# Optimization experiments

Hardware: AMD Instinct MI355X
Metric: run time of the kernel (lower is better)

## Reference

```python
import math
import jax, jax.numpy as jnp
import numpy as np

FS = 96000.0
N_BIQUADS = 16
HPF_FREQ_RANGE = (20.0, 500.0)
LPF_FREQ_RANGE = (5000.0, 20000.0)
SHELF_FREQ_RANGE = (50.0, 16000.0)
PEAK_FREQ_RANGE = (100.0, 15000.0)
Q_RANGE = (0.5, 16.0)
GAIN_RANGE = (-24.0, 24.0)
BROADBAND_RANGE = (-60.0, 0.0)


def _denorm_log(norm, lo, hi):
    return jnp.exp(math.log(lo) + norm * (math.log(hi) - math.log(lo)))


def _coef_highpass(fc, Q):
    w0 = 2.0 * math.pi * fc / FS
    alpha = jnp.sin(w0) / (2.0 * Q)
    c = jnp.cos(w0)
    b0 = (1 + c) / 2; b1 = -(1 + c); b2 = (1 + c) / 2
    a0 = 1 + alpha; a1 = -2 * c; a2 = 1 - alpha
    return b0 / a0, b1 / a0, b2 / a0, a1 / a0, a2 / a0


def _coef_lowpass(fc, Q):
    w0 = 2.0 * math.pi * fc / FS
    alpha = jnp.sin(w0) / (2.0 * Q)
    c = jnp.cos(w0)
    b0 = (1 - c) / 2; b1 = 1 - c; b2 = (1 - c) / 2
    a0 = 1 + alpha; a1 = -2 * c; a2 = 1 - alpha
    return b0 / a0, b1 / a0, b2 / a0, a1 / a0, a2 / a0


def _coef_lowshelf(fc, gain_db, Q):
    A = 10.0 ** (gain_db / 40.0)
    w0 = 2.0 * math.pi * fc / FS
    alpha = jnp.sin(w0) / (2.0 * Q)
    c = jnp.cos(w0)
    sA = jnp.sqrt(A)
    b0 = A * (A + 1 - (A - 1) * c + 2 * sA * alpha)
    b1 = 2 * A * (A - 1 - (A + 1) * c)
    b2 = A * (A + 1 - (A - 1) * c - 2 * sA * alpha)
    a0 = A + 1 + (A - 1) * c + 2 * sA * alpha
    a1 = -2 * (A - 1 + (A + 1) * c)
    a2 = A + 1 + (A - 1) * c - 2 * sA * alpha
    return b0 / a0, b1 / a0, b2 / a0, a1 / a0, a2 / a0


def _coef_highshelf(fc, gain_db, Q):
    A = 10.0 ** (gain_db / 40.0)
    w0 = 2.0 * math.pi * fc / FS
    alpha = jnp.sin(w0) / (2.0 * Q)
    c = jnp.cos(w0)
    sA = jnp.sqrt(A)
    b0 = A * (A + 1 + (A - 1) * c + 2 * sA * alpha)
    b1 = -2 * A * (A - 1 + (A + 1) * c)
    b2 = A * (A + 1 + (A - 1) * c - 2 * sA * alpha)
    a0 = A + 1 - (A - 1) * c + 2 * sA * alpha
    a1 = 2 * (A - 1 - (A + 1) * c)
    a2 = A + 1 - (A - 1) * c - 2 * sA * alpha
    return b0 / a0, b1 / a0, b2 / a0, a1 / a0, a2 / a0


def _coef_peak(fc, gain_db, Q):
    A = 10.0 ** (gain_db / 40.0)
    w0 = 2.0 * math.pi * fc / FS
    alpha = jnp.sin(w0) / (2.0 * Q)
    c = jnp.cos(w0)
    b0 = 1 + alpha * A; b1 = -2 * c; b2 = 1 - alpha * A
    a0 = 1 + alpha / A; a1 = -2 * c; a2 = 1 - alpha / A
    return b0 / a0, b1 / a0, b2 / a0, a1 / a0, a2 / a0


def _biquad(x, coefs):
    # x: (B, T); coefs: 5 arrays of shape (B,)
    b0, b1, b2, a1, a2 = coefs

    def step(carry, xt):  # xt: (B,)
        s1, s2 = carry
        y = b0 * xt + s1
        return (b1 * xt - a1 * y + s2, b2 * xt - a2 * y), y

    z = jnp.zeros(x.shape[0], x.dtype)
    _, ys = jax.lax.scan(step, (z, z), x.T)  # ys: (T, B)
    return ys.T


def _chain(audio, params):
    B = audio.shape[0]
    bp = params[:, :N_BIQUADS * 3].reshape(B, N_BIQUADS, 3)
    bb_lo, bb_hi = BROADBAND_RANGE
    in_db = bb_lo + params[:, -2] * (bb_hi - bb_lo)
    out_db = bb_lo + params[:, -1] * (bb_hi - bb_lo)
    x = audio * (10.0 ** (in_db / 20.0))[:, None]

    for i in range(N_BIQUADS):
        fn, gn, qn = bp[:, i, 0], bp[:, i, 1], bp[:, i, 2]
        Q = _denorm_log(qn, *Q_RANGE)
        gain = GAIN_RANGE[0] + gn * (GAIN_RANGE[1] - GAIN_RANGE[0])
        if i == 0:  # HPF
            coefs = _coef_highpass(_denorm_log(fn, *HPF_FREQ_RANGE), Q)
        elif i == 15:  # LPF
            coefs = _coef_lowpass(_denorm_log(fn, *LPF_FREQ_RANGE), Q)
        elif i == 1:  # low shelf
            coefs = _coef_lowshelf(_denorm_log(fn, *SHELF_FREQ_RANGE), gain, Q)
        elif i == 14:  # high shelf
            coefs = _coef_highshelf(_denorm_log(fn, *SHELF_FREQ_RANGE), gain, Q)
        else:  # peaking EQ
            coefs = _coef_peak(_denorm_log(fn, *PEAK_FREQ_RANGE), gain, Q)
        x = _biquad(x, coefs)

    return x * (10.0 ** (out_db / 20.0))[:, None]


def setup_inputs() -> dict:
    key = jax.random.key(0)
    k1, k2 = jax.random.split(key)
    audio = jax.random.normal(k1, (16, 262144), dtype=jnp.float32)
    params = jax.random.uniform(k2, (16, 50), dtype=jnp.float32)
    return {"audio": audio, "params": params}


def reference(audio, params):
    return _chain(audio, params)
```

## Files before the change

kernel.cpp:

```cpp
#include <hip/hip_runtime.h>
#include <math.h>

#define BATCH   16
#define T_LEN   262144
#define NB      16
#define L       64
#define GRP     64
#define SUB     16
#define CHAINS  4
#define NSUB    256
#define NSUP    16
#define NG      64
#define NCHUNK  4096

#define DPI 3.14159265358979323846264338327950288

#define OFF_COEF  0
#define OFF_A64   1536
#define OFF_A1K   17920
#define OFF_A16K  34304
#define OFF_QEND  50688
#define OFF_SARR  181760
#define OFF_P     312832

__device__ inline void stage_coefs(int i, double fn, double gn, double qn,
                                   double& B0, double& B1, double& B2,
                                   double& A1, double& A2) {
    const double FS = 96000.0;
    double Q    = exp(log(0.5) + qn * (log(16.0) - log(0.5)));
    double gain = -24.0 + gn * 48.0;
    double lo, hi;
    if (i == 0)            { lo = 20.0;   hi = 500.0;   }
    else if (i == 15)      { lo = 5000.0; hi = 20000.0; }
    else if (i == 1 || i == 14) { lo = 50.0; hi = 16000.0; }
    else                   { lo = 100.0;  hi = 15000.0; }
    double fc    = exp(log(lo) + fn * (log(hi) - log(lo)));
    double w0    = 2.0 * DPI * fc / FS;
    double alpha = sin(w0) / (2.0 * Q);
    double c     = cos(w0);
    double b0, b1, b2, a0, a1, a2;
    if (i == 0) {
        b0 = (1.0 + c) * 0.5; b1 = -(1.0 + c); b2 = (1.0 + c) * 0.5;
        a0 = 1.0 + alpha; a1 = -2.0 * c; a2 = 1.0 - alpha;
    } else if (i == 15) {
        b0 = (1.0 - c) * 0.5; b1 = 1.0 - c; b2 = (1.0 - c) * 0.5;
        a0 = 1.0 + alpha; a1 = -2.0 * c; a2 = 1.0 - alpha;
    } else if (i == 1) {
        double A = pow(10.0, gain / 40.0), sA = sqrt(A);
        b0 = A * ((A + 1.0) - (A - 1.0) * c + 2.0 * sA * alpha);
        b1 = 2.0 * A * ((A - 1.0) - (A + 1.0) * c);
        b2 = A * ((A + 1.0) - (A - 1.0) * c - 2.0 * sA * alpha);
        a0 = (A + 1.0) + (A - 1.0) * c + 2.0 * sA * alpha;
        a1 = -2.0 * ((A - 1.0) + (A + 1.0) * c);
        a2 = (A + 1.0) + (A - 1.0) * c - 2.0 * sA * alpha;
    } else if (i == 14) {
        double A = pow(10.0, gain / 40.0), sA = sqrt(A);
        b0 = A * ((A + 1.0) + (A - 1.0) * c + 2.0 * sA * alpha);
        b1 = -2.0 * A * ((A - 1.0) + (A + 1.0) * c);
        b2 = A * ((A + 1.0) + (A - 1.0) * c - 2.0 * sA * alpha);
        a0 = (A + 1.0) - (A - 1.0) * c + 2.0 * sA * alpha;
        a1 = 2.0 * ((A - 1.0) - (A + 1.0) * c);
        a2 = (A + 1.0) - (A - 1.0) * c - 2.0 * sA * alpha;
    } else {
        double A = pow(10.0, gain / 40.0);
        b0 = 1.0 + alpha * A; b1 = -2.0 * c; b2 = 1.0 - alpha * A;
        a0 = 1.0 + alpha / A; a1 = -2.0 * c; a2 = 1.0 - alpha / A;
    }
    B0 = b0 / a0; B1 = b1 / a0; B2 = b2 / a0; A1 = a1 / a0; A2 = a2 / a0;
}

__global__ __launch_bounds__(256) void k0_setup(const float* __restrict__ params,
                                                float* __restrict__ coefs,
                                                float* __restrict__ A64,
                                                float* __restrict__ A1K,
                                                float* __restrict__ A16K) {
    int b = blockIdx.x;
    int t = threadIdx.x;
    __shared__ double cf[NB][5];
    __shared__ double M1[32 * 32];
    __shared__ double M2[32 * 32];

    if (t < NB) {
        double B0, B1, B2, A1, A2;
        stage_coefs(t, (double)params[b * 50 + t * 3 + 0],
                       (double)params[b * 50 + t * 3 + 1],
                       (double)params[b * 50 + t * 3 + 2], B0, B1, B2, A1, A2);
        float f0 = (float)B0, f1 = (float)B1, f2 = (float)B2, f3 = (float)A1, f4 = (float)A2;
        cf[t][0] = (double)f0; cf[t][1] = (double)f1; cf[t][2] = (double)f2;
        cf[t][3] = (double)f3; cf[t][4] = (double)f4;
        float* cp = coefs + b * 96 + t * 5;
        cp[0] = f0; cp[1] = f1; cp[2] = f2; cp[3] = f3; cp[4] = f4;
    }
    if (t == NB) {
        double indb = -60.0 + (double)params[b * 50 + 48] * 60.0;
        coefs[b * 96 + 80] = (float)pow(10.0, indb / 20.0);
    }
    if (t == NB + 1) {
        double outdb = -60.0 + (double)params[b * 50 + 49] * 60.0;
        coefs[b * 96 + 81] = (float)pow(10.0, outdb / 20.0);
    }
    __syncthreads();

    if (t < 32) {
        double s1[NB], s2[NB];
#pragma unroll
        for (int i = 0; i < NB; i++) {
            s1[i] = (t == 2 * i) ? 1.0 : 0.0;
            s2[i] = (t == 2 * i + 1) ? 1.0 : 0.0;
        }
        double u = 0.0;
#pragma unroll
        for (int i = 0; i < NB; i++) {
            double y  = cf[i][0] * u + s1[i];
            double n1 = cf[i][1] * u - cf[i][3] * y + s2[i];
            double n2 = cf[i][2] * u - cf[i][4] * y;
            s1[i] = n1; s2[i] = n2; u = y;
        }
#pragma unroll
        for (int i = 0; i < NB; i++) {
            M1[(2 * i) * 32 + t]     = s1[i];
            M1[(2 * i + 1) * 32 + t] = s2[i];
        }
    }
    __syncthreads();

    int c  = t & 31;
    int r0 = t >> 5;
    double* src = M1;
    double* dst = M2;
    for (int sq = 0; sq < 14; sq++) {
        double acc[4] = {0.0, 0.0, 0.0, 0.0};
        for (int k = 0; k < 32; k++) {
            double bv = src[k * 32 + c];
#pragma unroll
            for (int e = 0; e < 4; e++)
                acc[e] += src[(e * 8 + r0) * 32 + k] * bv;
        }
#pragma unroll
        for (int e = 0; e < 4; e++) dst[(e * 8 + r0) * 32 + c] = acc[e];
        __syncthreads();
        { double* tmp = src; src = dst; dst = tmp; }
        float* out_m = (sq == 5) ? A64 : (sq == 9) ? A1K : (sq == 13) ? A16K : nullptr;
        if (out_m) {
#pragma unroll
            for (int e = 0; e < 4; e++) {
                int idx = (e * 8 + r0) * 32 + c;
                out_m[b * 1024 + idx] = (float)src[idx];
            }
        }
        __syncthreads();
    }
}

__device__ __forceinline__ float mv_step_rl(const float* ar, float q, float addv) {
    int qi = __float_as_int(q);
    float qb[32];
#pragma unroll
    for (int t = 0; t < 32; t++)
        qb[t] = __int_as_float(__builtin_amdgcn_readlane(qi, t));
    float acc0 = addv, acc1 = 0.f;
#pragma unroll
    for (int t = 0; t < 32; t += 2) {
        acc0 = fmaf(ar[t], qb[t], acc0);
        acc1 = fmaf(ar[t + 1], qb[t + 1], acc1);
    }
    return acc0 + acc1;
}

__device__ __forceinline__ void load_row32(const float* base, int row, float* ar) {
    const float4* a4 = (const float4*)(base + row * 32);
#pragma unroll
    for (int j = 0; j < 8; j++) {
        float4 v = a4[j];
        ar[4 * j + 0] = v.x; ar[4 * j + 1] = v.y;
        ar[4 * j + 2] = v.z; ar[4 * j + 3] = v.w;
    }
}

__device__ __forceinline__ void biquad4(const float4& xc, float ing,
                                        const float* c0, const float* c1,
                                        const float* c2, const float* c3,
                                        const float* c4,
                                        float* s1, float* s2, float* ys) {
    float xs[4] = {xc.x, xc.y, xc.z, xc.w};
#pragma unroll
    for (int j = 0; j < 4; j++) {
        float u = ing * xs[j];
#pragma unroll
        for (int i = 0; i < NB; i++) {
            float y  = fmaf(c0[i], u, s1[i]);
            float n1 = fmaf(c1[i], u, s2[i]); n1 = fmaf(-c3[i], y, n1);
            float n2 = c2[i] * u;             n2 = fmaf(-c4[i], y, n2);
            s1[i] = n1; s2[i] = n2; u = y;
        }
        ys[j] = u;
    }
}

__global__ __launch_bounds__(64, 4) void k1_pass1(const float* __restrict__ audio,
                                                  const float* __restrict__ coefs,
                                                  const float* __restrict__ A64,
                                                  float* __restrict__ P,
                                                  float* __restrict__ Qend) {
    int blk   = blockIdx.x;
    int batch = blk >> 6;
    int grp   = blk & 63;
    int lane  = threadIdx.x;
    int row   = lane & 31;

    __shared__ float plds[GRP][33];

    const float* cf = coefs + batch * 96;
    float c0[NB], c1[NB], c2[NB], c3[NB], c4[NB];
#pragma unroll
    for (int i = 0; i < NB; i++) {
        c0[i] = cf[i * 5 + 0]; c1[i] = cf[i * 5 + 1]; c2[i] = cf[i * 5 + 2];
        c3[i] = cf[i * 5 + 3]; c4[i] = cf[i * 5 + 4];
    }
    float ing = cf[80];

    float s1[NB], s2[NB];
#pragma unroll
    for (int i = 0; i < NB; i++) { s1[i] = 0.f; s2[i] = 0.f; }

    const float4* xgv = (const float4*)(audio + (size_t)batch * T_LEN
                                        + ((size_t)grp * GRP + lane) * L);
    float ys[4];
    float4 xv = xgv[0];
#pragma unroll 1
    for (int tt = 0; tt < 15; tt++) {
        float4 xc = xv;
        xv = xgv[tt + 1];
        biquad4(xc, ing, c0, c1, c2, c3, c4, s1, s2, ys);
    }
    biquad4(xv, ing, c0, c1, c2, c3, c4, s1, s2, ys);

    {
        float* pb = P + ((size_t)(batch * NG + grp)) * 2048;
#pragma unroll
        for (int i = 0; i < NB; i++) {
            pb[(2 * i) * 64 + lane]     = s1[i];
            pb[(2 * i + 1) * 64 + lane] = s2[i];
        }
    }

#pragma unroll
    for (int i = 0; i < NB; i++) {
        plds[lane][2 * i]     = s1[i];
        plds[lane][2 * i + 1] = s2[i];
    }
    __syncthreads();

    float ar[32];
    load_row32(A64 + batch * 1024, row, ar);
    float q0 = 0.f, q1 = 0.f, q2 = 0.f, q3 = 0.f;
#pragma unroll 1
    for (int j = 0; j < SUB; j++) {
        float p0 = plds[0 * SUB + j][row];
        float p1 = plds[1 * SUB + j][row];
        float p2 = plds[2 * SUB + j][row];
        float p3 = plds[3 * SUB + j][row];
        q0 = mv_step_rl(ar, q0, p0);
        q1 = mv_step_rl(ar, q1, p1);
        q2 = mv_step_rl(ar, q2, p2);
        q3 = mv_step_rl(ar, q3, p3);
    }
    if (lane < 32) {
        float* qe = Qend + ((size_t)(batch * NSUB + grp * CHAINS)) * 32 + row;
        qe[0] = q0; qe[32] = q1; qe[64] = q2; qe[96] = q3;
    }
}

__global__ __launch_bounds__(256, 1) void k2_combine(const float* __restrict__ A1K,
                                                     const float* __restrict__ A16K,
                                                     const float* __restrict__ Qend,
                                                     float* __restrict__ Sarr) {
    int batch = blockIdx.x;
    int tid   = threadIdx.x;
    int wave  = tid >> 6;
    int lane  = tid & 63;
    int row   = lane & 31;

    __shared__ float qe[NSUB][32];
    __shared__ float qs[NSUP][32];
    __shared__ float ss[NSUP][32];

    {
        const float4* src4 = (const float4*)(Qend + (size_t)batch * NSUB * 32);
        float4* dst4 = (float4*)&qe[0][0];
        for (int i = tid; i < NSUB * 32 / 4; i += 256) dst4[i] = src4[i];
    }
    float ar1k[32];
    load_row32(A1K + batch * 1024, row, ar1k);
    __syncthreads();

    int s0i = wave * 4;
    {
        float q0 = 0.f, q1 = 0.f, q2 = 0.f, q3 = 0.f;
#pragma unroll 1
        for (int j = 0; j < 16; j++) {
            float p0 = qe[(s0i + 0) * 16 + j][row];
            float p1 = qe[(s0i + 1) * 16 + j][row];
            float p2 = qe[(s0i + 2) * 16 + j][row];
            float p3 = qe[(s0i + 3) * 16 + j][row];
            q0 = mv_step_rl(ar1k, q0, p0);
            q1 = mv_step_rl(ar1k, q1, p1);
            q2 = mv_step_rl(ar1k, q2, p2);
            q3 = mv_step_rl(ar1k, q3, p3);
        }
        if (lane < 32) {
            qs[s0i + 0][row] = q0; qs[s0i + 1][row] = q1;
            qs[s0i + 2][row] = q2; qs[s0i + 3][row] = q3;
        }
    }
    __syncthreads();

    if (wave == 0) {
        float ark[32];
        load_row32(A16K + batch * 1024, row, ark);
        float S = 0.f;
#pragma unroll 1
        for (int s = 0; s < NSUP; s++) {
            if (lane < 32) ss[s][row] = S;
            float addv = qs[s][row];
            S = mv_step_rl(ark, S, addv);
        }
    }
    __syncthreads();

    {
        float q0 = ss[s0i + 0][row];
        float q1 = ss[s0i + 1][row];
        float q2 = ss[s0i + 2][row];
        float q3 = ss[s0i + 3][row];
#pragma unroll 1
        for (int j = 0; j < 16; j++) {
            if (lane < 32) {
                Sarr[((size_t)(batch * NSUB + (s0i + 0) * 16 + j)) * 32 + row] = q0;
                Sarr[((size_t)(batch * NSUB + (s0i + 1) * 16 + j)) * 32 + row] = q1;
                Sarr[((size_t)(batch * NSUB + (s0i + 2) * 16 + j)) * 32 + row] = q2;
                Sarr[((size_t)(batch * NSUB + (s0i + 3) * 16 + j)) * 32 + row] = q3;
            }
            float p0 = qe[(s0i + 0) * 16 + j][row];
            float p1 = qe[(s0i + 1) * 16 + j][row];
            float p2 = qe[(s0i + 2) * 16 + j][row];
            float p3 = qe[(s0i + 3) * 16 + j][row];
            q0 = mv_step_rl(ar1k, q0, p0);
            q1 = mv_step_rl(ar1k, q1, p1);
            q2 = mv_step_rl(ar1k, q2, p2);
            q3 = mv_step_rl(ar1k, q3, p3);
        }
    }
}

__global__ __launch_bounds__(64, 4) void k3_pass2(const float* __restrict__ audio,
                                                  const float* __restrict__ coefs,
                                                  const float* __restrict__ A64,
                                                  const float* __restrict__ P,
                                                  const float* __restrict__ Sarr,
                                                  float* __restrict__ out) {
    int blk   = blockIdx.x;
    int batch = blk >> 6;
    int grp   = blk & 63;
    int lane  = threadIdx.x;
    int row   = lane & 31;

    __shared__ float plds[GRP][33];

    {
        const float* pb = P + ((size_t)(batch * NG + grp)) * 2048;
        float pv[32];
#pragma unroll
        for (int s = 0; s < 32; s++) pv[s] = pb[s * 64 + lane];
#pragma unroll
        for (int s = 0; s < 32; s++) plds[lane][s] = pv[s];
    }
    __syncthreads();

    {
        float ar[32];
        load_row32(A64 + batch * 1024, row, ar);
        const float* sp = Sarr + ((size_t)(batch * NSUB + grp * CHAINS)) * 32 + row;
        float q0 = sp[0], q1 = sp[32], q2 = sp[64], q3 = sp[96];
#pragma unroll 1
        for (int j = 0; j < SUB; j++) {
            float p0 = plds[0 * SUB + j][row];
            float p1 = plds[1 * SUB + j][row];
            float p2 = plds[2 * SUB + j][row];
            float p3 = plds[3 * SUB + j][row];
            if (lane < 32) {
                plds[0 * SUB + j][row] = q0;
                plds[1 * SUB + j][row] = q1;
                plds[2 * SUB + j][row] = q2;
                plds[3 * SUB + j][row] = q3;
            }
            q0 = mv_step_rl(ar, q0, p0);
            q1 = mv_step_rl(ar, q1, p1);
            q2 = mv_step_rl(ar, q2, p2);
            q3 = mv_step_rl(ar, q3, p3);
        }
    }
    __syncthreads();

    const float* cf = coefs + batch * 96;
    float c0[NB], c1[NB], c2[NB], c3[NB], c4[NB];
#pragma unroll
    for (int i = 0; i < NB; i++) {
        c0[i] = cf[i * 5 + 0]; c1[i] = cf[i * 5 + 1]; c2[i] = cf[i * 5 + 2];
        c3[i] = cf[i * 5 + 3]; c4[i] = cf[i * 5 + 4];
    }
    float ing  = cf[80];
    float outg = cf[81];

    float s1[NB], s2[NB];
#pragma unroll
    for (int i = 0; i < NB; i++) {
        s1[i] = plds[lane][2 * i];
        s2[i] = plds[lane][2 * i + 1];
    }

    const float4* xgv = (const float4*)(audio + (size_t)batch * T_LEN
                                        + ((size_t)grp * GRP + lane) * L);
    float4* ogv = (float4*)(out + (size_t)batch * T_LEN
                            + ((size_t)grp * GRP + lane) * L);
    float ys[4];
    float4 xv = xgv[0];
#pragma unroll 1
    for (int tt = 0; tt < 15; tt++) {
        float4 xc = xv;
        xv = xgv[tt + 1];
        biquad4(xc, ing, c0, c1, c2, c3, c4, s1, s2, ys);
        float4 yv; yv.x = outg * ys[0]; yv.y = outg * ys[1];
        yv.z = outg * ys[2]; yv.w = outg * ys[3];
        ogv[tt] = yv;
    }
    biquad4(xv, ing, c0, c1, c2, c3, c4, s1, s2, ys);
    {
        float4 yv; yv.x = outg * ys[0]; yv.y = outg * ys[1];
        yv.z = outg * ys[2]; yv.w = outg * ys[3];
        ogv[15] = yv;
    }
}

extern "C" void kernel_launch(void* const* d_in, const int* in_sizes, int n_in,
                              void* d_out, int out_size, void* d_ws, size_t ws_size,
                              hipStream_t stream) {
    const float* audio  = (const float*)d_in[0];
    const float* params = (const float*)d_in[1];
    float* out = (float*)d_out;
    float* ws  = (float*)d_ws;

    float* coefs = ws + OFF_COEF;
    float* A64   = ws + OFF_A64;
    float* A1K   = ws + OFF_A1K;
    float* A16K  = ws + OFF_A16K;
    float* Qend  = ws + OFF_QEND;
    float* Sarr  = ws + OFF_SARR;
    float* P     = ws + OFF_P;

    k0_setup<<<BATCH, 256, 0, stream>>>(params, coefs, A64, A1K, A16K);
    k1_pass1<<<BATCH * NG, 64, 0, stream>>>(audio, coefs, A64, P, Qend);
    k2_combine<<<BATCH, 256, 0, stream>>>(A1K, A16K, Qend, Sarr);
    k3_pass2<<<BATCH * NG, 64, 0, stream>>>(audio, coefs, A64, P, Sarr, out);
}
```

Baseline: 154.4 us.

## Fuse pass1, combine and pass2 into one cooperative kernel with grid sync

Replaces the three-kernel scan (pass1, combine, pass2) with a single cooperative kernel of 256 blocks of 4 waves. Each wave keeps its chunk-end states in registers and LDS, so the P and Qend/Sarr round trips through global memory go away. The hierarchical carry propagation now uses block-local LDS plus two grid.sync barriers across super-chunks. It removes two kernel launches and the intermediate state traffic. In exchange it depends on cooperative launch, and the grid barriers serialize on a single block per batch doing the super-level scan.

```diff
diff --git a/kernel.cpp b/kernel.cpp
--- a/kernel.cpp
+++ b/kernel.cpp
@@ -1,5 +1,8 @@
 #include <hip/hip_runtime.h>
+#include <hip/hip_cooperative_groups.h>
 #include <math.h>
+
+namespace cg = cooperative_groups;
 
 #define BATCH   16
 #define T_LEN   262144
@@ -7,11 +10,7 @@
 #define L       64
 #define GRP     64
 #define SUB     16
-#define CHAINS  4
-#define NSUB    256
 #define NSUP    16
-#define NG      64
-#define NCHUNK  4096
 
 #define DPI 3.14159265358979323846264338327950288
 
@@ -19,9 +18,8 @@
 #define OFF_A64   1536
 #define OFF_A1K   17920
 #define OFF_A16K  34304
-#define OFF_QEND  50688
-#define OFF_SARR  181760
-#define OFF_P     312832
+#define OFF_QSUP  50688
+#define OFF_SSUP  58880
 
 __device__ inline void stage_coefs(int i, double fn, double gn, double qn,
                                    double& B0, double& B1, double& B2,
@@ -197,18 +195,26 @@
     }
 }
 
-__global__ __launch_bounds__(64, 4) void k1_pass1(const float* __restrict__ audio,
-                                                  const float* __restrict__ coefs,
-                                                  const float* __restrict__ A64,
-                                                  float* __restrict__ P,
-                                                  float* __restrict__ Qend) {
-    int blk   = blockIdx.x;
-    int batch = blk >> 6;
-    int grp   = blk & 63;
-    int lane  = threadIdx.x;
+__global__ __launch_bounds__(256, 1) void kfused(const float* __restrict__ audio,
+                                                 const float* __restrict__ coefs,
+                                                 const float* __restrict__ A64,
+                                                 const float* __restrict__ A1K,
+                                                 const float* __restrict__ A16K,
+                                                 float* __restrict__ qsupg,
+                                                 float* __restrict__ ssupg,
+                                                 float* __restrict__ out) {
+    cg::grid_group grid = cg::this_grid();
+    int tid   = threadIdx.x;
+    int w     = tid >> 6;
+    int lane  = tid & 63;
     int row   = lane & 31;
-
-    __shared__ float plds[GRP][33];
+    int batch = blockIdx.x >> 4;
+    int sup   = blockIdx.x & 15;
+    int grp   = sup * 4 + w;
+
+    __shared__ float plds[4][GRP][33];
+    __shared__ float qend_l[16][32];
+    __shared__ float ssub_l[16][32];
 
     const float* cf = coefs + batch * 96;
     float c0[NB], c1[NB], c2[NB], c3[NB], c4[NB];
@@ -217,7 +223,8 @@
         c0[i] = cf[i * 5 + 0]; c1[i] = cf[i * 5 + 1]; c2[i] = cf[i * 5 + 2];
         c3[i] = cf[i * 5 + 3]; c4[i] = cf[i * 5 + 4];
     }
-    float ing = cf[80];
+    float ing  = cf[80];
+    float outg = cf[81];
 
     float s1[NB], s2[NB];
 #pragma unroll
@@ -226,173 +233,108 @@
     const float4* xgv = (const float4*)(audio + (size_t)batch * T_LEN
                                         + ((size_t)grp * GRP + lane) * L);
     float ys[4];
-    float4 xv = xgv[0];
-#pragma unroll 1
-    for (int tt = 0; tt < 15; tt++) {
-        float4 xc = xv;
-        xv = xgv[tt + 1];
-        biquad4(xc, ing, c0, c1, c2, c3, c4, s1, s2, ys);
-    }
-    biquad4(xv, ing, c0, c1, c2, c3, c4, s1, s2, ys);
-
     {
-        float* pb = P + ((size_t)(batch * NG + grp)) * 2048;
-#pragma unroll
-        for (int i = 0; i < NB; i++) {
-            pb[(2 * i) * 64 + lane]     = s1[i];
-            pb[(2 * i + 1) * 64 + lane] = s2[i];
-        }
-    }
-
+        float4 xv = xgv[0];
+#pragma unroll 1
+        for (int tt = 0; tt < 15; tt++) {
+            float4 xc = xv;
+            xv = xgv[tt + 1];
+            biquad4(xc, ing, c0, c1, c2, c3, c4, s1, s2, ys);
+        }
+        biquad4(xv, ing, c0, c1, c2, c3, c4, s1, s2, ys);
+    }
 #pragma unroll
     for (int i = 0; i < NB; i++) {
-        plds[lane][2 * i]     = s1[i];
-        plds[lane][2 * i + 1] = s2[i];
-    }
-    __syncthreads();
-
-    float ar[32];
-    load_row32(A64 + batch * 1024, row, ar);
-    float q0 = 0.f, q1 = 0.f, q2 = 0.f, q3 = 0.f;
-#pragma unroll 1
-    for (int j = 0; j < SUB; j++) {
-        float p0 = plds[0 * SUB + j][row];
-        float p1 = plds[1 * SUB + j][row];
-        float p2 = plds[2 * SUB + j][row];
-        float p3 = plds[3 * SUB + j][row];
-        q0 = mv_step_rl(ar, q0, p0);
-        q1 = mv_step_rl(ar, q1, p1);
-        q2 = mv_step_rl(ar, q2, p2);
-        q3 = mv_step_rl(ar, q3, p3);
-    }
-    if (lane < 32) {
-        float* qe = Qend + ((size_t)(batch * NSUB + grp * CHAINS)) * 32 + row;
-        qe[0] = q0; qe[32] = q1; qe[64] = q2; qe[96] = q3;
-    }
-}
-
-__global__ __launch_bounds__(256, 1) void k2_combine(const float* __restrict__ A1K,
-                                                     const float* __restrict__ A16K,
-                                                     const float* __restrict__ Qend,
-                                                     float* __restrict__ Sarr) {
-    int batch = blockIdx.x;
-    int tid   = threadIdx.x;
-    int wave  = tid >> 6;
-    int lane  = tid & 63;
-    int row   = lane & 31;
-
-    __shared__ float qe[NSUB][32];
-    __shared__ float qs[NSUP][32];
-    __shared__ float ss[NSUP][32];
-
-    {
-        const float4* src4 = (const float4*)(Qend + (size_t)batch * NSUB * 32);
-        float4* dst4 = (float4*)&qe[0][0];
-        for (int i = tid; i < NSUB * 32 / 4; i += 256) dst4[i] = src4[i];
-    }
-    float ar1k[32];
-    load_row32(A1K + batch * 1024, row, ar1k);
-    __syncthreads();
-
-    int s0i = wave * 4;
-    {
-        float q0 = 0.f, q1 = 0.f, q2 = 0.f, q3 = 0.f;
-#pragma unroll 1
-        for (int j = 0; j < 16; j++) {
-            float p0 = qe[(s0i + 0) * 16 + j][row];
-            float p1 = qe[(s0i + 1) * 16 + j][row];
-            float p2 = qe[(s0i + 2) * 16 + j][row];
-            float p3 = qe[(s0i + 3) * 16 + j][row];
-            q0 = mv_step_rl(ar1k, q0, p0);
-            q1 = mv_step_rl(ar1k, q1, p1);
-            q2 = mv_step_rl(ar1k, q2, p2);
-            q3 = mv_step_rl(ar1k, q3, p3);
-        }
-        if (lane < 32) {
-            qs[s0i + 0][row] = q0; qs[s0i + 1][row] = q1;
-            qs[s0i + 2][row] = q2; qs[s0i + 3][row] = q3;
-        }
-    }
-    __syncthreads();
-
-    if (wave == 0) {
-        float ark[32];
-        load_row32(A16K + batch * 1024, row, ark);
-        float S = 0.f;
-#pragma unroll 1
-        for (int s = 0; s < NSUP; s++) {
-            if (lane < 32) ss[s][row] = S;
-            float addv = qs[s][row];
-            S = mv_step_rl(ark, S, addv);
-        }
-    }
-    __syncthreads();
-
-    {
-        float q0 = ss[s0i + 0][row];
-        float q1 = ss[s0i + 1][row];
-        float q2 = ss[s0i + 2][row];
-        float q3 = ss[s0i + 3][row];
-#pragma unroll 1
-        for (int j = 0; j < 16; j++) {
-            if (lane < 32) {
-                Sarr[((size_t)(batch * NSUB + (s0i + 0) * 16 + j)) * 32 + row] = q0;
-                Sarr[((size_t)(batch * NSUB + (s0i + 1) * 16 + j)) * 32 + row] = q1;
-                Sarr[((size_t)(batch * NSUB + (s0i + 2) * 16 + j)) * 32 + row] = q2;
-                Sarr[((size_t)(batch * NSUB + (s0i + 3) * 16 + j)) * 32 + row] = q3;
-            }
-            float p0 = qe[(s0i + 0) * 16 + j][row];
-            float p1 = qe[(s0i + 1) * 16 + j][row];
-            float p2 = qe[(s0i + 2) * 16 + j][row];
-            float p3 = qe[(s0i + 3) * 16 + j][row];
-            q0 = mv_step_rl(ar1k, q0, p0);
-            q1 = mv_step_rl(ar1k, q1, p1);
-            q2 = mv_step_rl(ar1k, q2, p2);
-            q3 = mv_step_rl(ar1k, q3, p3);
-        }
-    }
-}
-
-__global__ __launch_bounds__(64, 4) void k3_pass2(const float* __restrict__ audio,
-                                                  const float* __restrict__ coefs,
-                                                  const float* __restrict__ A64,
-                                                  const float* __restrict__ P,
-                                                  const float* __restrict__ Sarr,
-                                                  float* __restrict__ out) {
-    int blk   = blockIdx.x;
-    int batch = blk >> 6;
-    int grp   = blk & 63;
-    int lane  = threadIdx.x;
-    int row   = lane & 31;
-
-    __shared__ float plds[GRP][33];
-
-    {
-        const float* pb = P + ((size_t)(batch * NG + grp)) * 2048;
-        float pv[32];
-#pragma unroll
-        for (int s = 0; s < 32; s++) pv[s] = pb[s * 64 + lane];
-#pragma unroll
-        for (int s = 0; s < 32; s++) plds[lane][s] = pv[s];
+        plds[w][lane][2 * i]     = s1[i];
+        plds[w][lane][2 * i + 1] = s2[i];
     }
     __syncthreads();
 
     {
         float ar[32];
         load_row32(A64 + batch * 1024, row, ar);
-        const float* sp = Sarr + ((size_t)(batch * NSUB + grp * CHAINS)) * 32 + row;
-        float q0 = sp[0], q1 = sp[32], q2 = sp[64], q3 = sp[96];
+        float q0 = 0.f, q1 = 0.f, q2 = 0.f, q3 = 0.f;
 #pragma unroll 1
         for (int j = 0; j < SUB; j++) {
-            float p0 = plds[0 * SUB + j][row];
-            float p1 = plds[1 * SUB + j][row];
-            float p2 = plds[2 * SUB + j][row];
-            float p3 = plds[3 * SUB + j][row];
+            float p0 = plds[w][0 * SUB + j][row];
+            float p1 = plds[w][1 * SUB + j][row];
+            float p2 = plds[w][2 * SUB + j][row];
+            float p3 = plds[w][3 * SUB + j][row];
+            q0 = mv_step_rl(ar, q0, p0);
+            q1 = mv_step_rl(ar, q1, p1);
+            q2 = mv_step_rl(ar, q2, p2);
+            q3 = mv_step_rl(ar, q3, p3);
+        }
+        if (lane < 32) {
+            qend_l[w * 4 + 0][row] = q0;
+            qend_l[w * 4 + 1][row] = q1;
+            qend_l[w * 4 + 2][row] = q2;
+            qend_l[w * 4 + 3][row] = q3;
+        }
+    }
+    __syncthreads();
+
+    if (w == 0) {
+        float ar1k[32];
+        load_row32(A1K + batch * 1024, row, ar1k);
+        float S = 0.f;
+#pragma unroll 1
+        for (int s = 0; s < 16; s++)
+            S = mv_step_rl(ar1k, S, qend_l[s][row]);
+        if (lane < 32)
+            qsupg[((size_t)(batch * NSUP + sup)) * 32 + row] = S;
+    }
+    __threadfence();
+    grid.sync();
+
+    if (sup == 0 && w == 0) {
+        float ark[32];
+        load_row32(A16K + batch * 1024, row, ark);
+        float qv[16];
+#pragma unroll
+        for (int s = 0; s < 16; s++)
+            qv[s] = qsupg[((size_t)(batch * NSUP + s)) * 32 + row];
+        float S = 0.f;
+#pragma unroll 1
+        for (int s = 0; s < 16; s++) {
+            if (lane < 32)
+                ssupg[((size_t)(batch * NSUP + s)) * 32 + row] = S;
+            S = mv_step_rl(ark, S, qv[s]);
+        }
+    }
+    __threadfence();
+    grid.sync();
+
+    if (w == 0) {
+        float ar1k[32];
+        load_row32(A1K + batch * 1024, row, ar1k);
+        float Sq = ssupg[((size_t)(batch * NSUP + sup)) * 32 + row];
+#pragma unroll 1
+        for (int j = 0; j < 16; j++) {
+            if (lane < 32) ssub_l[j][row] = Sq;
+            Sq = mv_step_rl(ar1k, Sq, qend_l[j][row]);
+        }
+    }
+    __syncthreads();
+
+    {
+        float ar[32];
+        load_row32(A64 + batch * 1024, row, ar);
+        float q0 = ssub_l[w * 4 + 0][row];
+        float q1 = ssub_l[w * 4 + 1][row];
+        float q2 = ssub_l[w * 4 + 2][row];
+        float q3 = ssub_l[w * 4 + 3][row];
+#pragma unroll 1
+        for (int j = 0; j < SUB; j++) {
+            float p0 = plds[w][0 * SUB + j][row];
+            float p1 = plds[w][1 * SUB + j][row];
+            float p2 = plds[w][2 * SUB + j][row];
+            float p3 = plds[w][3 * SUB + j][row];
             if (lane < 32) {
-                plds[0 * SUB + j][row] = q0;
-                plds[1 * SUB + j][row] = q1;
-                plds[2 * SUB + j][row] = q2;
-                plds[3 * SUB + j][row] = q3;
+                plds[w][0 * SUB + j][row] = q0;
+                plds[w][1 * SUB + j][row] = q1;
+                plds[w][2 * SUB + j][row] = q2;
+                plds[w][3 * SUB + j][row] = q3;
             }
             q0 = mv_step_rl(ar, q0, p0);
             q1 = mv_step_rl(ar, q1, p1);
@@ -402,40 +344,25 @@
     }
     __syncthreads();
 
-    const float* cf = coefs + batch * 96;
-    float c0[NB], c1[NB], c2[NB], c3[NB], c4[NB];
 #pragma unroll
     for (int i = 0; i < NB; i++) {
-        c0[i] = cf[i * 5 + 0]; c1[i] = cf[i * 5 + 1]; c2[i] = cf[i * 5 + 2];
-        c3[i] = cf[i * 5 + 3]; c4[i] = cf[i * 5 + 4];
-    }
-    float ing  = cf[80];
-    float outg = cf[81];
-
-    float s1[NB], s2[NB];
-#pragma unroll
-    for (int i = 0; i < NB; i++) {
-        s1[i] = plds[lane][2 * i];
-        s2[i] = plds[lane][2 * i + 1];
-    }
-
-    const float4* xgv = (const float4*)(audio + (size_t)batch * T_LEN
-                                        + ((size_t)grp * GRP + lane) * L);
-    float4* ogv = (float4*)(out + (size_t)batch * T_LEN
-                            + ((size_t)grp * GRP + lane) * L);
-    float ys[4];
-    float4 xv = xgv[0];
-#pragma unroll 1
-    for (int tt = 0; tt < 15; tt++) {
-        float4 xc = xv;
-        xv = xgv[tt + 1];
-        biquad4(xc, ing, c0, c1, c2, c3, c4, s1, s2, ys);
-        float4 yv; yv.x = outg * ys[0]; yv.y = outg * ys[1];
-        yv.z = outg * ys[2]; yv.w = outg * ys[3];
-        ogv[tt] = yv;
-    }
-    biquad4(xv, ing, c0, c1, c2, c3, c4, s1, s2, ys);
+        s1[i] = plds[w][lane][2 * i];
+        s2[i] = plds[w][lane][2 * i + 1];
+    }
     {
+        float4* ogv = (float4*)(out + (size_t)batch * T_LEN
+                                + ((size_t)grp * GRP + lane) * L);
+        float4 xv = xgv[0];
+#pragma unroll 1
+        for (int tt = 0; tt < 15; tt++) {
+            float4 xc = xv;
+            xv = xgv[tt + 1];
+            biquad4(xc, ing, c0, c1, c2, c3, c4, s1, s2, ys);
+            float4 yv; yv.x = outg * ys[0]; yv.y = outg * ys[1];
+            yv.z = outg * ys[2]; yv.w = outg * ys[3];
+            ogv[tt] = yv;
+        }
+        biquad4(xv, ing, c0, c1, c2, c3, c4, s1, s2, ys);
         float4 yv; yv.x = outg * ys[0]; yv.y = outg * ys[1];
         yv.z = outg * ys[2]; yv.w = outg * ys[3];
         ogv[15] = yv;
@@ -454,12 +381,13 @@
     float* A64   = ws + OFF_A64;
     float* A1K   = ws + OFF_A1K;
     float* A16K  = ws + OFF_A16K;
-    float* Qend  = ws + OFF_QEND;
-    float* Sarr  = ws + OFF_SARR;
-    float* P     = ws + OFF_P;
+    float* qsupg = ws + OFF_QSUP;
+    float* ssupg = ws + OFF_SSUP;
 
     k0_setup<<<BATCH, 256, 0, stream>>>(params, coefs, A64, A1K, A16K);
-    k1_pass1<<<BATCH * NG, 64, 0, stream>>>(audio, coefs, A64, P, Qend);
-    k2_combine<<<BATCH, 256, 0, stream>>>(A1K, A16K, Qend, Sarr);
-    k3_pass2<<<BATCH * NG, 64, 0, stream>>>(audio, coefs, A64, P, Sarr, out);
-}
+
+    void* kargs[] = {(void*)&audio, (void*)&coefs, (void*)&A64, (void*)&A1K,
+                     (void*)&A16K, (void*)&qsupg, (void*)&ssupg, (void*)&out};
+    hipLaunchCooperativeKernel((const void*)kfused, dim3(256), dim3(256),
+                               kargs, 0, stream);
+}
```

New measurement: 241.3 us. 1.56x slower.

## Process samples in pairs through the biquad chain and stage output via LDS

Applied to the files above, without the earlier changes.

Replaces the per-sample biquad cascade with a two-sample block update that uses a precomputed combined coefficient (b1 - a1*b0). This shortens the serial dependency chain per stage, at the cost of extra registers and some FMA reordering that can change rounding. The pass-2 output is now staged through LDS so that global stores are coalesced across lanes. Launch bounds drop to one block per SIMD, which allows more registers per thread but lowers occupancy.

```diff
diff --git a/kernel.cpp b/kernel.cpp
--- a/kernel.cpp
+++ b/kernel.cpp
@@ -11,17 +11,16 @@
 #define NSUB    256
 #define NSUP    16
 #define NG      64
-#define NCHUNK  4096
 
 #define DPI 3.14159265358979323846264338327950288
 
 #define OFF_COEF  0
-#define OFF_A64   1536
-#define OFF_A1K   17920
-#define OFF_A16K  34304
-#define OFF_QEND  50688
-#define OFF_SARR  181760
-#define OFF_P     312832
+#define OFF_A64   1792
+#define OFF_A1K   18176
+#define OFF_A16K  34560
+#define OFF_QEND  50944
+#define OFF_SARR  182016
+#define OFF_P     313088
 
 __device__ inline void stage_coefs(int i, double fn, double gn, double qn,
                                    double& B0, double& B1, double& B2,
@@ -88,16 +87,17 @@
         float f0 = (float)B0, f1 = (float)B1, f2 = (float)B2, f3 = (float)A1, f4 = (float)A2;
         cf[t][0] = (double)f0; cf[t][1] = (double)f1; cf[t][2] = (double)f2;
         cf[t][3] = (double)f3; cf[t][4] = (double)f4;
-        float* cp = coefs + b * 96 + t * 5;
-        cp[0] = f0; cp[1] = f1; cp[2] = f2; cp[3] = f3; cp[4] = f4;
+        float gg = (float)((double)f1 - (double)f3 * (double)f0);
+        float* cp = coefs + b * 112 + t * 6;
+        cp[0] = f0; cp[1] = gg; cp[2] = f1; cp[3] = f2; cp[4] = f3; cp[5] = f4;
     }
     if (t == NB) {
         double indb = -60.0 + (double)params[b * 50 + 48] * 60.0;
-        coefs[b * 96 + 80] = (float)pow(10.0, indb / 20.0);
+        coefs[b * 112 + 96] = (float)pow(10.0, indb / 20.0);
     }
     if (t == NB + 1) {
         double outdb = -60.0 + (double)params[b * 50 + 49] * 60.0;
-        coefs[b * 96 + 81] = (float)pow(10.0, outdb / 20.0);
+        coefs[b * 112 + 97] = (float)pow(10.0, outdb / 20.0);
     }
     __syncthreads();
 
@@ -177,27 +177,24 @@
     }
 }
 
-__device__ __forceinline__ void biquad4(const float4& xc, float ing,
-                                        const float* c0, const float* c1,
-                                        const float* c2, const float* c3,
-                                        const float* c4,
-                                        float* s1, float* s2, float* ys) {
-    float xs[4] = {xc.x, xc.y, xc.z, xc.w};
-#pragma unroll
-    for (int j = 0; j < 4; j++) {
-        float u = ing * xs[j];
-#pragma unroll
-        for (int i = 0; i < NB; i++) {
-            float y  = fmaf(c0[i], u, s1[i]);
-            float n1 = fmaf(c1[i], u, s2[i]); n1 = fmaf(-c3[i], y, n1);
-            float n2 = c2[i] * u;             n2 = fmaf(-c4[i], y, n2);
-            s1[i] = n1; s2[i] = n2; u = y;
-        }
-        ys[j] = u;
-    }
-}
-
-__global__ __launch_bounds__(64, 4) void k1_pass1(const float* __restrict__ audio,
+__device__ __forceinline__ void biquad_pair(float& u0, float& u1,
+                                            const float* cb0, const float* cg,
+                                            const float* cb1, const float* cb2,
+                                            const float* ca1, const float* ca2,
+                                            float* s1, float* s2) {
+#pragma unroll
+    for (int i = 0; i < NB; i++) {
+        float t  = fmaf(-ca1[i], s1[i], s2[i]);
+        float y0 = fmaf(cb0[i], u0, s1[i]);
+        float y1 = fmaf(cb0[i], u1, fmaf(cg[i], u0, t));
+        float w  = fmaf(cb2[i], u0, cb1[i] * u1);
+        s1[i] = fmaf(-ca1[i], y1, fmaf(-ca2[i], y0, w));
+        s2[i] = fmaf(-ca2[i], y1, cb2[i] * u1);
+        u0 = y0; u1 = y1;
+    }
+}
+
+__global__ __launch_bounds__(64, 1) void k1_pass1(const float* __restrict__ audio,
                                                   const float* __restrict__ coefs,
                                                   const float* __restrict__ A64,
                                                   float* __restrict__ P,
@@ -210,14 +207,14 @@
 
     __shared__ float plds[GRP][33];
 
-    const float* cf = coefs + batch * 96;
-    float c0[NB], c1[NB], c2[NB], c3[NB], c4[NB];
+    const float* cf = coefs + batch * 112;
+    float cb0[NB], cg[NB], cb1[NB], cb2[NB], ca1[NB], ca2[NB];
 #pragma unroll
     for (int i = 0; i < NB; i++) {
-        c0[i] = cf[i * 5 + 0]; c1[i] = cf[i * 5 + 1]; c2[i] = cf[i * 5 + 2];
-        c3[i] = cf[i * 5 + 3]; c4[i] = cf[i * 5 + 4];
-    }
-    float ing = cf[80];
+        cb0[i] = cf[i * 6 + 0]; cg[i]  = cf[i * 6 + 1]; cb1[i] = cf[i * 6 + 2];
+        cb2[i] = cf[i * 6 + 3]; ca1[i] = cf[i * 6 + 4]; ca2[i] = cf[i * 6 + 5];
+    }
+    float ing = cf[96];
 
     float s1[NB], s2[NB];
 #pragma unroll
@@ -225,15 +222,16 @@
 
     const float4* xgv = (const float4*)(audio + (size_t)batch * T_LEN
                                         + ((size_t)grp * GRP + lane) * L);
-    float ys[4];
     float4 xv = xgv[0];
 #pragma unroll 1
-    for (int tt = 0; tt < 15; tt++) {
+    for (int tt = 0; tt < 16; tt++) {
         float4 xc = xv;
-        xv = xgv[tt + 1];
-        biquad4(xc, ing, c0, c1, c2, c3, c4, s1, s2, ys);
-    }
-    biquad4(xv, ing, c0, c1, c2, c3, c4, s1, s2, ys);
+        if (tt < 15) xv = xgv[tt + 1];
+        float u0 = ing * xc.x, u1 = ing * xc.y;
+        biquad_pair(u0, u1, cb0, cg, cb1, cb2, ca1, ca2, s1, s2);
+        u0 = ing * xc.z; u1 = ing * xc.w;
+        biquad_pair(u0, u1, cb0, cg, cb1, cb2, ca1, ca2, s1, s2);
+    }
 
     {
         float* pb = P + ((size_t)(batch * NG + grp)) * 2048;
@@ -353,7 +351,7 @@
     }
 }
 
-__global__ __launch_bounds__(64, 4) void k3_pass2(const float* __restrict__ audio,
+__global__ __launch_bounds__(64, 1) void k3_pass2(const float* __restrict__ audio,
                                                   const float* __restrict__ coefs,
                                                   const float* __restrict__ A64,
                                                   const float* __restrict__ P,
@@ -402,15 +400,15 @@
     }
     __syncthreads();
 
-    const float* cf = coefs + batch * 96;
-    float c0[NB], c1[NB], c2[NB], c3[NB], c4[NB];
+    const float* cf = coefs + batch * 112;
+    float cb0[NB], cg[NB], cb1[NB], cb2[NB], ca1[NB], ca2[NB];
 #pragma unroll
     for (int i = 0; i < NB; i++) {
-        c0[i] = cf[i * 5 + 0]; c1[i] = cf[i * 5 + 1]; c2[i] = cf[i * 5 + 2];
-        c3[i] = cf[i * 5 + 3]; c4[i] = cf[i * 5 + 4];
-    }
-    float ing  = cf[80];
-    float outg = cf[81];
+        cb0[i] = cf[i * 6 + 0]; cg[i]  = cf[i * 6 + 1]; cb1[i] = cf[i * 6 + 2];
+        cb2[i] = cf[i * 6 + 3]; ca1[i] = cf[i * 6 + 4]; ca2[i] = cf[i * 6 + 5];
+    }
+    float ing  = cf[96];
+    float outg = cf[97];
 
     float s1[NB], s2[NB];
 #pragma unroll
@@ -418,27 +416,38 @@
         s1[i] = plds[lane][2 * i];
         s2[i] = plds[lane][2 * i + 1];
     }
+    __syncthreads();
+
+    float* olds = &plds[0][0];
 
     const float4* xgv = (const float4*)(audio + (size_t)batch * T_LEN
                                         + ((size_t)grp * GRP + lane) * L);
-    float4* ogv = (float4*)(out + (size_t)batch * T_LEN
-                            + ((size_t)grp * GRP + lane) * L);
-    float ys[4];
+    float4* ob4 = (float4*)(out + (size_t)batch * T_LEN + (size_t)grp * (GRP * L));
+
     float4 xv = xgv[0];
 #pragma unroll 1
-    for (int tt = 0; tt < 15; tt++) {
+    for (int tt = 0; tt < 16; tt++) {
         float4 xc = xv;
-        xv = xgv[tt + 1];
-        biquad4(xc, ing, c0, c1, c2, c3, c4, s1, s2, ys);
-        float4 yv; yv.x = outg * ys[0]; yv.y = outg * ys[1];
-        yv.z = outg * ys[2]; yv.w = outg * ys[3];
-        ogv[tt] = yv;
-    }
-    biquad4(xv, ing, c0, c1, c2, c3, c4, s1, s2, ys);
-    {
-        float4 yv; yv.x = outg * ys[0]; yv.y = outg * ys[1];
-        yv.z = outg * ys[2]; yv.w = outg * ys[3];
-        ogv[15] = yv;
+        if (tt < 15) xv = xgv[tt + 1];
+        float u0 = ing * xc.x, u1 = ing * xc.y;
+        biquad_pair(u0, u1, cb0, cg, cb1, cb2, ca1, ca2, s1, s2);
+        olds[lane * 20 + (tt & 3) * 4 + 0] = outg * u0;
+        olds[lane * 20 + (tt & 3) * 4 + 1] = outg * u1;
+        float v0 = ing * xc.z, v1 = ing * xc.w;
+        biquad_pair(v0, v1, cb0, cg, cb1, cb2, ca1, ca2, s1, s2);
+        olds[lane * 20 + (tt & 3) * 4 + 2] = outg * v0;
+        olds[lane * 20 + (tt & 3) * 4 + 3] = outg * v1;
+
+        if ((tt & 3) == 3) {
+            int b4 = tt >> 2;
+#pragma unroll
+            for (int it = 0; it < 4; it++) {
+                int f  = it * 64 + lane;
+                int ch = f >> 2, s4 = f & 3;
+                float4 v = *(const float4*)&olds[ch * 20 + s4 * 4];
+                ob4[ch * 16 + b4 * 4 + s4] = v;
+            }
+        }
     }
 }
 
```

Measured after the change: 166.1 us. 7.5% more time.
